# Kernel optimization log

Hardware: AMD Instinct MI355X
Metric: run time of the kernel (lower is better)

Reference implementation:

```python
import jax, jax.numpy as jnp
import numpy as np

# Sizes (match input_specs)
B = 50                 # number of CRN graphs in the batch
NS_PER, NR_PER = 2000, 4000
N_S, N_R = B * NS_PER, B * NR_PER   # 100k species, 200k reactions total
E = 1_000_000          # bipartite edges
D = 128                # d_model
L = 2                  # n_layers
N_TYPES, P_DIM = 16, 8
MAX_SPECIES_IDX = 2000


def setup_inputs() -> dict:
    key = jax.random.key(0)
    ks = jax.random.split(key, 12)
    inp = {
        "species_indices": jax.random.randint(ks[0], (N_S,), 0, MAX_SPECIES_IDX, dtype=jnp.int32),
        "is_external": jax.random.randint(ks[1], (N_S,), 0, 2, dtype=jnp.int32),
        "propensity_type_ids": jax.random.randint(ks[2], (N_R,), 0, N_TYPES, dtype=jnp.int32),
        "propensity_params": jax.random.normal(ks[3], (N_R, P_DIM), dtype=jnp.float32),
        "edge_species": jax.random.randint(ks[4], (E,), 0, N_S, dtype=jnp.int32),
        "edge_reaction": jax.random.randint(ks[5], (E,), 0, N_R, dtype=jnp.int32),
        # contiguous per-graph segment ids (graphs are equal-sized)
        "species_batch": jnp.repeat(jnp.arange(B, dtype=jnp.int32), NS_PER),
        "reaction_batch": jnp.repeat(jnp.arange(B, dtype=jnp.int32), NR_PER),
        # learned parameters
        "species_table": jax.random.normal(ks[6], (MAX_SPECIES_IDX, D), dtype=jnp.float32) * 0.02,
        "external_table": jax.random.normal(ks[7], (2, D), dtype=jnp.float32) * 0.02,
        "type_table": jax.random.normal(ks[8], (N_TYPES, D), dtype=jnp.float32) * 0.02,
        "W_param": jax.random.normal(ks[9], (P_DIM, D), dtype=jnp.float32) * 0.1,
        "b_param": jnp.zeros((D,), dtype=jnp.float32),
        # per-layer message-passing weights: concat([h, msg]) -> d
        "Wr": jax.random.normal(ks[10], (L, 2 * D, D), dtype=jnp.float32) * 0.05,
        "br": jnp.zeros((L, D), dtype=jnp.float32),
        "Ws": jax.random.normal(ks[11], (L, 2 * D, D), dtype=jnp.float32) * 0.05,
        "bs": jnp.zeros((L, D), dtype=jnp.float32),
    }
    return inp


def reference(species_indices, is_external, propensity_type_ids, propensity_params,
              edge_species, edge_reaction, species_batch, reaction_batch,
              species_table, external_table, type_table, W_param, b_param,
              Wr, br, Ws, bs):
    # Initial embeddings
    h_s = species_table[species_indices] + external_table[is_external]          # (N_S, D)
    h_r = type_table[propensity_type_ids] + propensity_params @ W_param + b_param  # (N_R, D)

    n_s, n_r = h_s.shape[0], h_r.shape[0]
    # Alternating bipartite sum message passing (SumMessagePassingLayer)
    for l in range(Wr.shape[0]):
        m_r = jax.ops.segment_sum(h_s[edge_species], edge_reaction, num_segments=n_r)
        h_r = jax.nn.relu(jnp.concatenate([h_r, m_r], axis=-1) @ Wr[l] + br[l])
        m_s = jax.ops.segment_sum(h_r[edge_reaction], edge_species, num_segments=n_s)
        h_s = jax.nn.relu(jnp.concatenate([h_s, m_s], axis=-1) @ Ws[l] + bs[l])

    # Segment-mean pooling per graph (index_add then divide by counts)
    pooled_s = jax.ops.segment_sum(h_s, species_batch, num_segments=B) / float(NS_PER)
    pooled_r = jax.ops.segment_sum(h_r, reaction_batch, num_segments=B) / float(NR_PER)
    context = jnp.concatenate([pooled_s, pooled_r], axis=-1)  # (B, 2D); dropout p=0 -> identity
    return context
```

## Files before the change

kernel.cpp:

```cpp
#include <hip/hip_runtime.h>
#include <stdint.h>

#define NS 100000
#define NR 200000
#define EE 1000000
#define DD 128
#define NB 50
#define NSP 2000
#define NRP 4000
#define BSH 10
#define NBR 196
#define NBS 98
#define CHUNK 8192

typedef short bf16x8 __attribute__((ext_vector_type(8)));
typedef float f32x4 __attribute__((ext_vector_type(4)));
typedef unsigned u32x4 __attribute__((ext_vector_type(4)));
typedef unsigned u32x2 __attribute__((ext_vector_type(2)));

__device__ __forceinline__ unsigned short f2bf(float f){
  unsigned u = __float_as_uint(f);
  u = (u + 0x7FFFu + ((u >> 16) & 1u)) >> 16;
  return (unsigned short)u;
}
__device__ __forceinline__ float bf2f(unsigned short s){
  return __uint_as_float(((unsigned)s) << 16);
}
__device__ __forceinline__ unsigned packbf(float a, float b){
  return (unsigned)f2bf(a) | ((unsigned)f2bf(b) << 16);
}
__device__ __forceinline__ float bflo(unsigned p){ return __uint_as_float(p << 16); }
__device__ __forceinline__ float bfhi(unsigned p){ return __uint_as_float(p & 0xFFFF0000u); }

__global__ void pack_w(const float* __restrict__ Wr, const float* __restrict__ Ws,
                       unsigned short* __restrict__ Wp){
  int g = blockIdx.x*256 + threadIdx.x;
  if (g >= 4*32768) return;
  int j = g & 7; int rest = g >> 3;
  int lane = rest & 63; rest >>= 6;
  int ks = rest & 7; rest >>= 3;
  int ct = rest & 7; int mat = rest >> 3;
  int k  = ks*32 + (lane >> 4)*8 + j;
  int cc = ct*16 + (lane & 15);
  const float* src = (mat < 2) ? (Wr + (size_t)mat*256*DD) : (Ws + (size_t)(mat-2)*256*DD);
  Wp[g] = f2bf(src[(size_t)k*DD + cc]);
}

__global__ __launch_bounds__(256) void init_all(const int* __restrict__ si, const int* __restrict__ ext,
        const int* __restrict__ tid, const float* __restrict__ pp,
        const float* __restrict__ st, const float* __restrict__ et, const float* __restrict__ tt,
        const float* __restrict__ Wpar, const float* __restrict__ bpar,
        unsigned short* __restrict__ hs, unsigned short* __restrict__ hr){
  int g = blockIdx.x*256 + threadIdx.x;
  int row = g >> 4, colb = (g & 15) * 8;
  if (row < NS){
    const float* a = st + (size_t)si[row]*DD + colb;
    const float* b = et + (size_t)ext[row]*DD + colb;
    float4 x0 = ((const float4*)a)[0], x1 = ((const float4*)a)[1];
    float4 y0 = ((const float4*)b)[0], y1 = ((const float4*)b)[1];
    u32x4 o;
    o.x = packbf(x0.x+y0.x, x0.y+y0.y);
    o.y = packbf(x0.z+y0.z, x0.w+y0.w);
    o.z = packbf(x1.x+y1.x, x1.y+y1.y);
    o.w = packbf(x1.z+y1.z, x1.w+y1.w);
    *(u32x4*)(hs + (size_t)row*DD + colb) = o;
  } else {
    int r = row - NS;
    const float* tb = tt + (size_t)tid[r]*DD + colb;
    float4 a0 = ((const float4*)tb)[0], a1 = ((const float4*)tb)[1];
    float4 b0 = ((const float4*)(bpar+colb))[0], b1 = ((const float4*)(bpar+colb))[1];
    a0.x += b0.x; a0.y += b0.y; a0.z += b0.z; a0.w += b0.w;
    a1.x += b1.x; a1.y += b1.y; a1.z += b1.z; a1.w += b1.w;
    const float* pr = pp + (size_t)r*8;
    float4 p0 = ((const float4*)pr)[0], p1 = ((const float4*)pr)[1];
    float w[8] = {p0.x,p0.y,p0.z,p0.w,p1.x,p1.y,p1.z,p1.w};
    #pragma unroll
    for (int p = 0; p < 8; p++){
      float4 w0 = ((const float4*)(Wpar + p*DD + colb))[0];
      float4 w1 = ((const float4*)(Wpar + p*DD + colb))[1];
      a0.x += w[p]*w0.x; a0.y += w[p]*w0.y; a0.z += w[p]*w0.z; a0.w += w[p]*w0.w;
      a1.x += w[p]*w1.x; a1.y += w[p]*w1.y; a1.z += w[p]*w1.z; a1.w += w[p]*w1.w;
    }
    u32x4 o;
    o.x = packbf(a0.x, a0.y); o.y = packbf(a0.z, a0.w);
    o.z = packbf(a1.x, a1.y); o.w = packbf(a1.z, a1.w);
    *(u32x4*)(hr + (size_t)r*DD + colb) = o;
  }
}

__global__ __launch_bounds__(256) void bucket_hist(const int* __restrict__ er, const int* __restrict__ es,
                                                   int* __restrict__ gcnt){
  __shared__ int cnt[NBR + NBS];
  int t = threadIdx.x;
  for (int j = t; j < NBR + NBS; j += 256) cnt[j] = 0;
  __syncthreads();
  long i0 = (long)blockIdx.x * 2048;
  for (int j = t; j < 2048; j += 256){
    long i = i0 + j;
    if (i < EE){
      atomicAdd(&cnt[er[i] >> BSH], 1);
      atomicAdd(&cnt[NBR + (es[i] >> BSH)], 1);
    }
  }
  __syncthreads();
  for (int j = t; j < NBR + NBS; j += 256)
    if (cnt[j]) atomicAdd(&gcnt[j], cnt[j]);
}

__global__ __launch_bounds__(256) void bucket_scan(const int* __restrict__ gcnt,
        int* __restrict__ bktOffR, int* __restrict__ bktOffS,
        int* __restrict__ gCurR, int* __restrict__ gCurS){
  __shared__ int a[256];
  int t = threadIdx.x;
  int own = (t < NBR) ? gcnt[t] : 0;
  a[t] = own; __syncthreads();
  for (int d = 1; d < 256; d <<= 1){
    int x = (t >= d) ? a[t-d] : 0;
    __syncthreads(); a[t] += x; __syncthreads();
  }
  if (t < NBR){ int v = a[t] - own; bktOffR[t] = v; gCurR[t] = v; }
  if (t == 0) bktOffR[NBR] = EE;
  __syncthreads();
  own = (t < NBS) ? gcnt[NBR + t] : 0;
  a[t] = own; __syncthreads();
  for (int d = 1; d < 256; d <<= 1){
    int x = (t >= d) ? a[t-d] : 0;
    __syncthreads(); a[t] += x; __syncthreads();
  }
  if (t < NBS){ int v = a[t] - own; bktOffS[t] = v; gCurS[t] = v; }
  if (t == 0) bktOffS[NBS] = EE;
}

__global__ __launch_bounds__(256) void bin_edges(const int* __restrict__ er, const int* __restrict__ es,
        int* __restrict__ gCurR, int* __restrict__ gCurS,
        unsigned* __restrict__ recR, unsigned* __restrict__ recS){
  __shared__ unsigned stage[CHUNK];
  __shared__ unsigned char stageb[CHUNK];
  __shared__ int cnt[256], scn[256], pref[256], gbase[256], lcur[256];
  int t = threadIdx.x;
  int side = blockIdx.y;
  const int* dest = side ? es : er;
  const int* srca = side ? er : es;
  int* gCur = side ? gCurS : gCurR;
  unsigned* rec = side ? recS : recR;
  int nbkt = side ? NBS : NBR;
  long i0 = (long)blockIdx.x * CHUNK;
  int n = (EE - i0 < CHUNK) ? (int)(EE - i0) : CHUNK;
  cnt[t] = 0;
  __syncthreads();
  for (int j = t; j < n; j += 256)
    atomicAdd(&cnt[dest[i0 + j] >> BSH], 1);
  __syncthreads();
  scn[t] = cnt[t];
  __syncthreads();
  for (int d = 1; d < 256; d <<= 1){
    int x = (t >= d) ? scn[t-d] : 0;
    __syncthreads(); scn[t] += x; __syncthreads();
  }
  pref[t] = scn[t] - cnt[t];
  lcur[t] = scn[t] - cnt[t];
  if (t < nbkt && cnt[t] > 0) gbase[t] = atomicAdd(&gCur[t], cnt[t]);
  __syncthreads();
  for (int j = t; j < n; j += 256){
    int d = dest[i0 + j];
    int s = srca[i0 + j];
    int b = d >> BSH;
    int p = atomicAdd(&lcur[b], 1);
    stage[p] = ((unsigned)(d - (b << BSH)) << 18) | (unsigned)s;
    stageb[p] = (unsigned char)b;
  }
  __syncthreads();
  for (int e = t; e < n; e += 256){
    int b = stageb[e];
    rec[gbase[b] + (e - pref[b])] = stage[e];
  }
}

__global__ __launch_bounds__(256) void build_csr(const unsigned* __restrict__ recR, const unsigned* __restrict__ recS,
        const int* __restrict__ bktOffR, const int* __restrict__ bktOffS,
        unsigned* __restrict__ csrR, unsigned* __restrict__ csrS,
        int* __restrict__ offsR, int* __restrict__ offsS){
  __shared__ int hist[1024], pref[1024], cur[1024], ws[256];
  int t = threadIdx.x;
  int bb = blockIdx.x;
  const unsigned* rec; const int* bktOff; unsigned* csr; int* offs; int N;
  if (bb < NBR){ rec = recR; bktOff = bktOffR; csr = csrR; offs = offsR; N = NR; }
  else { bb -= NBR; rec = recS; bktOff = bktOffS; csr = csrS; offs = offsS; N = NS; }
  int d0 = bb << BSH;
  int base = bktOff[bb], cnt_ = bktOff[bb+1] - base;
  #pragma unroll
  for (int j = 0; j < 4; j++) hist[t*4+j] = 0;
  __syncthreads();
  for (int e = t; e < cnt_; e += 256)
    atomicAdd(&hist[rec[base + e] >> 18], 1);
  __syncthreads();
  int s = 0, h[4];
  #pragma unroll
  for (int j = 0; j < 4; j++){ h[j] = hist[t*4+j]; s += h[j]; }
  ws[t] = s;
  __syncthreads();
  for (int d = 1; d < 256; d <<= 1){
    int x = (t >= d) ? ws[t-d] : 0;
    __syncthreads(); ws[t] += x; __syncthreads();
  }
  int run = ws[t] - s;
  #pragma unroll
  for (int j = 0; j < 4; j++){ pref[t*4+j] = run; cur[t*4+j] = base + run; run += h[j]; }
  __syncthreads();
  int DPB = N - d0; if (DPB > 1024) DPB = 1024;
  #pragma unroll
  for (int j = 0; j < 4; j++){
    int i = t*4 + j;
    if (i < DPB) offs[d0 + i] = base + pref[i];
  }
  if (t == 0 && d0 + DPB == N) offs[N] = EE;
  __syncthreads();
  for (int e = t; e < cnt_; e += 256){
    unsigned r = rec[base + e];
    int pos = atomicAdd(&cur[r >> 18], 1);
    csr[pos] = (((r >> 18) & 31u) << 26) | ((r & 0x3FFFFu) << 8);
  }
}

__global__ __launch_bounds__(256) void fused_layer(
        const unsigned short* __restrict__ gsrc,
        const unsigned short* __restrict__ hself,
        const int* __restrict__ offs, const unsigned* __restrict__ csr,
        const unsigned short* __restrict__ Wp, const float* __restrict__ bias,
        unsigned short* __restrict__ hout)
{
  __shared__ unsigned short msgT[32*DD];
  int t = threadIdx.x;
  int lane = t & 63;
  int w = t >> 6;
  int quad = lane >> 4, rlo = lane & 15;
  int row0 = blockIdx.x * 32;

  for (int i = t; i < 2048; i += 256) ((unsigned*)msgT)[i] = 0u;
  __syncthreads();

  {
    int rbeg = row0 + w*8;
    int k  = __builtin_amdgcn_readfirstlane(offs[rbeg]);
    int ke = __builtin_amdgcn_readfirstlane(offs[rbeg + 8]);
    int c16 = lane >> 2, sub4 = lane & 3;
    const char* gbase = (const char*)gsrc;
    float a0 = 0.f, a1 = 0.f;
    int cur = -1;
    unsigned rc[8]; unsigned pv[8];
    if (k < ke){
      #pragma unroll
      for (int i = 0; i < 8; i++){
        int kk = (k + i < ke) ? (k + i) : (ke - 1);
        rc[i] = (unsigned)__builtin_amdgcn_readfirstlane(csr[kk]);
      }
      #pragma unroll
      for (int i = 0; i < 8; i++)
        pv[i] = *(const unsigned*)(gbase + (rc[i] & 0x03FFFF00u) + lane*4);
      while (k < ke){
        unsigned rc2[8], pv2[8];
        int kn = k + 8;
        #pragma unroll
        for (int i = 0; i < 8; i++){
          int kk = (kn + i < ke) ? (kn + i) : (ke - 1);
          rc2[i] = (unsigned)__builtin_amdgcn_readfirstlane(csr[kk]);
        }
        #pragma unroll
        for (int i = 0; i < 8; i++)
          pv2[i] = *(const unsigned*)(gbase + (rc2[i] & 0x03FFFF00u) + lane*4);
        #pragma unroll
        for (int i = 0; i < 8; i++){
          if (k + i < ke){
            int dl = (int)(rc[i] >> 26);
            if (dl != cur){
              if (cur >= 0)
                *(unsigned*)(msgT + cur*DD + ((c16 ^ (cur & 7)) << 3) + (sub4 << 1)) = packbf(a0, a1);
              a0 = 0.f; a1 = 0.f;
              cur = dl;
            }
            a0 += bflo(pv[i]); a1 += bfhi(pv[i]);
          }
        }
        #pragma unroll
        for (int i = 0; i < 8; i++){ rc[i] = rc2[i]; pv[i] = pv2[i]; }
        k = kn;
      }
      if (cur >= 0)
        *(unsigned*)(msgT + cur*DD + ((c16 ^ (cur & 7)) << 3) + (sub4 << 1)) = packbf(a0, a1);
    }
  }
  __syncthreads();

  int ct0 = w * 2;
  bf16x8 wf[16];
  #pragma unroll
  for (int ks = 0; ks < 8; ks++){
    wf[ks*2+0] = *(const bf16x8*)(Wp + (size_t)(((ct0+0)*8 + ks)*64 + lane) * 8);
    wf[ks*2+1] = *(const bf16x8*)(Wp + (size_t)(((ct0+1)*8 + ks)*64 + lane) * 8);
  }
  bf16x8 Hb0[4], Hb1[4];
  #pragma unroll
  for (int ks = 0; ks < 4; ks++){
    int kloc = ks*32 + quad*8;
    Hb0[ks] = *(const bf16x8*)(hself + (size_t)(row0 + rlo) * DD + kloc);
    Hb1[ks] = *(const bf16x8*)(hself + (size_t)(row0 + 16 + rlo) * DD + kloc);
  }
  bf16x8 Mb0[4], Mb1[4];
  #pragma unroll
  for (int ks2 = 0; ks2 < 4; ks2++){
    int c8 = ks2*4 + quad;
    int lr0 = rlo, lr1 = 16 + rlo;
    Mb0[ks2] = *(const bf16x8*)(msgT + lr0*DD + ((c8 ^ (lr0 & 7)) * 8));
    Mb1[ks2] = *(const bf16x8*)(msgT + lr1*DD + ((c8 ^ (lr1 & 7)) * 8));
  }

  f32x4 acc[2][2];
  #pragma unroll
  for (int i = 0; i < 2; i++)
    #pragma unroll
    for (int j = 0; j < 2; j++){ f32x4 z = {0.f,0.f,0.f,0.f}; acc[i][j] = z; }

  #pragma unroll
  for (int ks = 0; ks < 4; ks++){
    acc[0][0] = __builtin_amdgcn_mfma_f32_16x16x32_bf16(wf[ks*2+0], Hb0[ks], acc[0][0], 0, 0, 0);
    acc[0][1] = __builtin_amdgcn_mfma_f32_16x16x32_bf16(wf[ks*2+1], Hb0[ks], acc[0][1], 0, 0, 0);
    acc[1][0] = __builtin_amdgcn_mfma_f32_16x16x32_bf16(wf[ks*2+0], Hb1[ks], acc[1][0], 0, 0, 0);
    acc[1][1] = __builtin_amdgcn_mfma_f32_16x16x32_bf16(wf[ks*2+1], Hb1[ks], acc[1][1], 0, 0, 0);
  }
  #pragma unroll
  for (int ks2 = 0; ks2 < 4; ks2++){
    int ks = 4 + ks2;
    acc[0][0] = __builtin_amdgcn_mfma_f32_16x16x32_bf16(wf[ks*2+0], Mb0[ks2], acc[0][0], 0, 0, 0);
    acc[0][1] = __builtin_amdgcn_mfma_f32_16x16x32_bf16(wf[ks*2+1], Mb0[ks2], acc[0][1], 0, 0, 0);
    acc[1][0] = __builtin_amdgcn_mfma_f32_16x16x32_bf16(wf[ks*2+0], Mb1[ks2], acc[1][0], 0, 0, 0);
    acc[1][1] = __builtin_amdgcn_mfma_f32_16x16x32_bf16(wf[ks*2+1], Mb1[ks2], acc[1][1], 0, 0, 0);
  }

  #pragma unroll
  for (int c = 0; c < 2; c++){
    float4 bv = *(const float4*)(bias + (ct0+c)*16 + quad*4);
    #pragma unroll
    for (int rb = 0; rb < 2; rb++){
      int row = row0 + rb*16 + rlo;
      float v0 = acc[rb][c][0] + bv.x;
      float v1 = acc[rb][c][1] + bv.y;
      float v2 = acc[rb][c][2] + bv.z;
      float v3 = acc[rb][c][3] + bv.w;
      v0 = v0 > 0.f ? v0 : 0.f;
      v1 = v1 > 0.f ? v1 : 0.f;
      v2 = v2 > 0.f ? v2 : 0.f;
      v3 = v3 > 0.f ? v3 : 0.f;
      u32x2 o; o.x = packbf(v0, v1); o.y = packbf(v2, v3);
      *(u32x2*)(hout + (size_t)row*DD + (ct0+c)*16 + quad*4) = o;
    }
  }
}

__global__ __launch_bounds__(256) void pool(const unsigned short* __restrict__ hs,
        const unsigned short* __restrict__ hr, float* __restrict__ out){
  __shared__ float red[16][128];
  int b = blockIdx.x, part = blockIdx.y;
  int t = threadIdx.x;
  int rg = t >> 4, sub = t & 15;
  const unsigned short* src; int row0, outoff; float scale;
  if (part < 4){ src = hs; row0 = b*NSP + part*500; outoff = b*256; scale = 1.f/NSP; }
  else { src = hr; row0 = b*NRP + (part-4)*500; outoff = b*256 + 128; scale = 1.f/NRP; }
  float a0=0,a1=0,a2=0,a3=0,a4=0,a5=0,a6=0,a7=0;
  for (int r = rg; r < 500; r += 16){
    u32x4 p = *(const u32x4*)(src + (size_t)(row0+r)*DD + sub*8);
    a0 += bflo(p.x); a1 += bfhi(p.x);
    a2 += bflo(p.y); a3 += bfhi(p.y);
    a4 += bflo(p.z); a5 += bfhi(p.z);
    a6 += bflo(p.w); a7 += bfhi(p.w);
  }
  float* rr = &red[rg][sub*8];
  rr[0]=a0; rr[1]=a1; rr[2]=a2; rr[3]=a3; rr[4]=a4; rr[5]=a5; rr[6]=a6; rr[7]=a7;
  __syncthreads();
  if (t < 128){
    float s = 0.f;
    #pragma unroll
    for (int g = 0; g < 16; g++) s += red[g][t];
    atomicAdd(&out[outoff + t], s * scale);
  }
}

extern "C" void kernel_launch(void* const* d_in, const int* in_sizes, int n_in,
                              void* d_out, int out_size, void* d_ws, size_t ws_size,
                              hipStream_t stream)
{
  const int*   si   = (const int*)d_in[0];
  const int*   ext  = (const int*)d_in[1];
  const int*   tid  = (const int*)d_in[2];
  const float* pp   = (const float*)d_in[3];
  const int*   es   = (const int*)d_in[4];
  const int*   er   = (const int*)d_in[5];
  const float* st   = (const float*)d_in[8];
  const float* et   = (const float*)d_in[9];
  const float* tt   = (const float*)d_in[10];
  const float* Wpar = (const float*)d_in[11];
  const float* bpar = (const float*)d_in[12];
  const float* Wr   = (const float*)d_in[13];
  const float* br   = (const float*)d_in[14];
  const float* Ws   = (const float*)d_in[15];
  const float* bs   = (const float*)d_in[16];
  float* out = (float*)d_out;

  char* basep = (char*)d_ws; size_t off = 0;
  auto alloc = [&](size_t bytes)->char*{
    char* r = basep + off; off = (off + bytes + 255) & ~(size_t)255; return r;
  };
  unsigned short* hs0 = (unsigned short*)alloc((size_t)NS*DD*2);
  unsigned short* hs1 = (unsigned short*)alloc((size_t)NS*DD*2);
  unsigned short* hr0 = (unsigned short*)alloc((size_t)NR*DD*2);
  unsigned short* hr1 = (unsigned short*)alloc((size_t)NR*DD*2);
  unsigned short* Wp  = (unsigned short*)alloc((size_t)4*32768*2);
  int* offsR = (int*)alloc((size_t)(NR+1)*4);
  int* offsS = (int*)alloc((size_t)(NS+1)*4);
  unsigned* csrR = (unsigned*)alloc((size_t)EE*4);
  unsigned* csrS = (unsigned*)alloc((size_t)EE*4);
  int* gcnt   = (int*)alloc(2048);
  int* bktOffR= (int*)alloc(2048);
  int* bktOffS= (int*)alloc(2048);
  int* gCurR  = (int*)alloc(2048);
  int* gCurS  = (int*)alloc(2048);
  unsigned* recR = (unsigned*)hs1;
  unsigned* recS = (unsigned*)hr1;

  hipMemsetAsync(gcnt, 0, 2048, stream);
  hipMemsetAsync(d_out, 0, (size_t)out_size*4, stream);

  pack_w<<<512, 256, 0, stream>>>(Wr, Ws, Wp);
  init_all<<<(NS+NR)*16/256, 256, 0, stream>>>(si, ext, tid, pp, st, et, tt, Wpar, bpar, hs0, hr0);

  bucket_hist<<<(EE + 2047)/2048, 256, 0, stream>>>(er, es, gcnt);
  bucket_scan<<<1, 256, 0, stream>>>(gcnt, bktOffR, bktOffS, gCurR, gCurS);
  bin_edges<<<dim3((EE + CHUNK - 1)/CHUNK, 2), 256, 0, stream>>>(er, es, gCurR, gCurS, recR, recS);
  build_csr<<<NBR + NBS, 256, 0, stream>>>(recR, recS, bktOffR, bktOffS, csrR, csrS, offsR, offsS);

  fused_layer<<<NR/32, 256, 0, stream>>>(hs0, hr0, offsR, csrR, Wp + (size_t)0*32768, br + (size_t)0*DD, hr1);
  fused_layer<<<NS/32, 256, 0, stream>>>(hr1, hs0, offsS, csrS, Wp + (size_t)2*32768, bs + (size_t)0*DD, hs1);
  fused_layer<<<NR/32, 256, 0, stream>>>(hs1, hr1, offsR, csrR, Wp + (size_t)1*32768, br + (size_t)1*DD, hr0);
  fused_layer<<<NS/32, 256, 0, stream>>>(hr0, hs1, offsS, csrS, Wp + (size_t)3*32768, bs + (size_t)1*DD, hs0);

  pool<<<dim3(NB, 12), 256, 0, stream>>>(hs0, hr0, out);
}
```

Before: 463.2 us.

## Pad CSR rows to even length and gather two edges per wave

CSR construction is split into a histogram kernel, a serial pad-scan kernel and a scatter kernel. Each destination's edge list is padded to an even length with a dummy edge that points at an extra zeroed row appended to each feature buffer. In the fused layer, the two half-waves then load 8-byte slices from two different source rows at once and combine partial sums with a cross-half shuffle before writing to LDS. The goal is fewer loop iterations and wider gather loads. The cost is three extra launches, four small memsets, a single-threaded scan, and extra padded edges to gather.

```diff
diff --git a/kernel.cpp b/kernel.cpp
--- a/kernel.cpp
+++ b/kernel.cpp
@@ -22,9 +22,6 @@
   unsigned u = __float_as_uint(f);
   u = (u + 0x7FFFu + ((u >> 16) & 1u)) >> 16;
   return (unsigned short)u;
-}
-__device__ __forceinline__ float bf2f(unsigned short s){
-  return __uint_as_float(((unsigned)s) << 16);
 }
 __device__ __forceinline__ unsigned packbf(float a, float b){
   return (unsigned)f2bf(a) | ((unsigned)f2bf(b) << 16);
@@ -176,49 +173,89 @@
   }
 }
 
-__global__ __launch_bounds__(256) void build_csr(const unsigned* __restrict__ recR, const unsigned* __restrict__ recS,
+__global__ __launch_bounds__(256) void csr_hist(const unsigned* __restrict__ recR, const unsigned* __restrict__ recS,
         const int* __restrict__ bktOffR, const int* __restrict__ bktOffS,
-        unsigned* __restrict__ csrR, unsigned* __restrict__ csrS,
-        int* __restrict__ offsR, int* __restrict__ offsS){
-  __shared__ int hist[1024], pref[1024], cur[1024], ws[256];
-  int t = threadIdx.x;
-  int bb = blockIdx.x;
-  const unsigned* rec; const int* bktOff; unsigned* csr; int* offs; int N;
-  if (bb < NBR){ rec = recR; bktOff = bktOffR; csr = csrR; offs = offsR; N = NR; }
-  else { bb -= NBR; rec = recS; bktOff = bktOffS; csr = csrS; offs = offsS; N = NS; }
-  int d0 = bb << BSH;
-  int base = bktOff[bb], cnt_ = bktOff[bb+1] - base;
+        int* __restrict__ histBuf, int* __restrict__ gPad){
+  __shared__ int hist[1024]; __shared__ int ws[256];
+  int t = threadIdx.x; int bb = blockIdx.x;
+  const unsigned* rec; const int* bktOff; int lb;
+  if (bb < NBR){ rec = recR; bktOff = bktOffR; lb = bb; }
+  else { rec = recS; bktOff = bktOffS; lb = bb - NBR; }
+  int base = bktOff[lb], cnt_ = bktOff[lb+1] - base;
   #pragma unroll
   for (int j = 0; j < 4; j++) hist[t*4+j] = 0;
   __syncthreads();
   for (int e = t; e < cnt_; e += 256)
     atomicAdd(&hist[rec[base + e] >> 18], 1);
   __syncthreads();
-  int s = 0, h[4];
-  #pragma unroll
-  for (int j = 0; j < 4; j++){ h[j] = hist[t*4+j]; s += h[j]; }
-  ws[t] = s;
-  __syncthreads();
+  int s = 0;
+  #pragma unroll
+  for (int j = 0; j < 4; j++){
+    int h = hist[t*4+j];
+    histBuf[bb*1024 + t*4 + j] = h;
+    s += h + (h & 1);
+  }
+  ws[t] = s; __syncthreads();
   for (int d = 1; d < 256; d <<= 1){
     int x = (t >= d) ? ws[t-d] : 0;
     __syncthreads(); ws[t] += x; __syncthreads();
   }
-  int run = ws[t] - s;
-  #pragma unroll
-  for (int j = 0; j < 4; j++){ pref[t*4+j] = run; cur[t*4+j] = base + run; run += h[j]; }
-  __syncthreads();
+  if (t == 255) gPad[bb] = ws[255];
+}
+
+__global__ void padscan(const int* __restrict__ gPad, int* __restrict__ padBase){
+  if (threadIdx.x == 0 && blockIdx.x == 0){
+    int b = 0;
+    for (int i = 0; i < NBR; i++){ padBase[i] = b; b += gPad[i]; }
+    padBase[NBR] = b;
+    b = 0;
+    for (int i = 0; i < NBS; i++){ padBase[256 + i] = b; b += gPad[NBR + i]; }
+    padBase[256 + NBS] = b;
+  }
+}
+
+__global__ __launch_bounds__(256) void csr_scatter(const unsigned* __restrict__ recR, const unsigned* __restrict__ recS,
+        const int* __restrict__ bktOffR, const int* __restrict__ bktOffS,
+        const int* __restrict__ histBuf, const int* __restrict__ padBase,
+        unsigned* __restrict__ csrR, unsigned* __restrict__ csrS,
+        int* __restrict__ offsR, int* __restrict__ offsS){
+  __shared__ int cur[1024], ws[256];
+  int t = threadIdx.x; int bb = blockIdx.x;
+  const unsigned* rec; const int* bktOff; unsigned* csr; int* offs; int N, lb, pbase; unsigned zrow;
+  if (bb < NBR){ rec = recR; bktOff = bktOffR; csr = csrR; offs = offsR; N = NR; lb = bb;
+                 pbase = padBase[bb]; zrow = NS; }
+  else { lb = bb - NBR; rec = recS; bktOff = bktOffS; csr = csrS; offs = offsS; N = NS;
+         pbase = padBase[256 + lb]; zrow = NR; }
+  int d0 = lb << BSH;
+  int base = bktOff[lb], cnt_ = bktOff[lb+1] - base;
+  int h[4], s = 0;
+  #pragma unroll
+  for (int j = 0; j < 4; j++){ h[j] = histBuf[bb*1024 + t*4 + j]; s += h[j] + (h[j] & 1); }
+  ws[t] = s; __syncthreads();
+  for (int d = 1; d < 256; d <<= 1){
+    int x = (t >= d) ? ws[t-d] : 0;
+    __syncthreads(); ws[t] += x; __syncthreads();
+  }
+  int run = pbase + ws[t] - s;
   int DPB = N - d0; if (DPB > 1024) DPB = 1024;
   #pragma unroll
   for (int j = 0; j < 4; j++){
     int i = t*4 + j;
-    if (i < DPB) offs[d0 + i] = base + pref[i];
-  }
-  if (t == 0 && d0 + DPB == N) offs[N] = EE;
+    cur[i] = run;
+    if (i < DPB){
+      offs[d0 + i] = run;
+      if (h[j] & 1) csr[run + h[j]] = ((unsigned)(i & 31) << 26) | (zrow << 8);
+    }
+    run += h[j] + (h[j] & 1);
+  }
+  if (t == 0 && d0 + DPB == N)
+    offs[N] = (N == NR) ? padBase[NBR] : padBase[256 + NBS];
   __syncthreads();
   for (int e = t; e < cnt_; e += 256){
     unsigned r = rec[base + e];
-    int pos = atomicAdd(&cur[r >> 18], 1);
-    csr[pos] = (((r >> 18) & 31u) << 26) | ((r & 0x3FFFFu) << 8);
+    int dloc10 = r >> 18;
+    int pos = atomicAdd(&cur[dloc10], 1);
+    csr[pos] = ((unsigned)(dloc10 & 31) << 26) | ((r & 0x3FFFFu) << 8);
   }
 }
 
@@ -243,22 +280,37 @@
     int rbeg = row0 + w*8;
     int k  = __builtin_amdgcn_readfirstlane(offs[rbeg]);
     int ke = __builtin_amdgcn_readfirstlane(offs[rbeg + 8]);
-    int c16 = lane >> 2, sub4 = lane & 3;
+    int half = lane >> 5, col4 = lane & 31;
     const char* gbase = (const char*)gsrc;
-    float a0 = 0.f, a1 = 0.f;
+    float a0 = 0.f, a1 = 0.f, a2 = 0.f, a3 = 0.f;
     int cur = -1;
-    unsigned rc[8]; unsigned pv[8];
+
+    auto flushrow = [&](){
+      float s0 = a0 + __shfl_xor(a0, 32, 64);
+      float s1 = a1 + __shfl_xor(a1, 32, 64);
+      float s2 = a2 + __shfl_xor(a2, 32, 64);
+      float s3 = a3 + __shfl_xor(a3, 32, 64);
+      if (lane < 32){
+        u32x2 o; o.x = packbf(s0, s1); o.y = packbf(s2, s3);
+        *(u32x2*)(msgT + cur*DD + (((col4 >> 1) ^ (cur & 7)) * 8) + ((col4 & 1) * 4)) = o;
+      }
+      a0 = 0.f; a1 = 0.f; a2 = 0.f; a3 = 0.f;
+    };
+
     if (k < ke){
+      unsigned rc[8]; u32x2 pv[4];
       #pragma unroll
       for (int i = 0; i < 8; i++){
         int kk = (k + i < ke) ? (k + i) : (ke - 1);
         rc[i] = (unsigned)__builtin_amdgcn_readfirstlane(csr[kk]);
       }
       #pragma unroll
-      for (int i = 0; i < 8; i++)
-        pv[i] = *(const unsigned*)(gbase + (rc[i] & 0x03FFFF00u) + lane*4);
+      for (int j = 0; j < 4; j++){
+        unsigned rsel = half ? rc[2*j+1] : rc[2*j];
+        pv[j] = *(const u32x2*)(gbase + (rsel & 0x03FFFF00u) + col4*8);
+      }
       while (k < ke){
-        unsigned rc2[8], pv2[8];
+        unsigned rc2[8]; u32x2 pv2[4];
         int kn = k + 8;
         #pragma unroll
         for (int i = 0; i < 8; i++){
@@ -266,27 +318,29 @@
           rc2[i] = (unsigned)__builtin_amdgcn_readfirstlane(csr[kk]);
         }
         #pragma unroll
-        for (int i = 0; i < 8; i++)
-          pv2[i] = *(const unsigned*)(gbase + (rc2[i] & 0x03FFFF00u) + lane*4);
+        for (int j = 0; j < 4; j++){
+          unsigned rsel = half ? rc2[2*j+1] : rc2[2*j];
+          pv2[j] = *(const u32x2*)(gbase + (rsel & 0x03FFFF00u) + col4*8);
+        }
         #pragma unroll
-        for (int i = 0; i < 8; i++){
-          if (k + i < ke){
-            int dl = (int)(rc[i] >> 26);
+        for (int j = 0; j < 4; j++){
+          if (k + 2*j < ke){
+            int dl = (int)(rc[2*j] >> 26);
             if (dl != cur){
-              if (cur >= 0)
-                *(unsigned*)(msgT + cur*DD + ((c16 ^ (cur & 7)) << 3) + (sub4 << 1)) = packbf(a0, a1);
-              a0 = 0.f; a1 = 0.f;
+              if (cur >= 0) flushrow();
               cur = dl;
             }
-            a0 += bflo(pv[i]); a1 += bfhi(pv[i]);
+            a0 += bflo(pv[j].x); a1 += bfhi(pv[j].x);
+            a2 += bflo(pv[j].y); a3 += bfhi(pv[j].y);
           }
         }
         #pragma unroll
-        for (int i = 0; i < 8; i++){ rc[i] = rc2[i]; pv[i] = pv2[i]; }
+        for (int i = 0; i < 8; i++) rc[i] = rc2[i];
+        #pragma unroll
+        for (int j = 0; j < 4; j++) pv[j] = pv2[j];
         k = kn;
       }
-      if (cur >= 0)
-        *(unsigned*)(msgT + cur*DD + ((c16 ^ (cur & 7)) << 3) + (sub4 << 1)) = packbf(a0, a1);
+      if (cur >= 0) flushrow();
     }
   }
   __syncthreads();
@@ -409,25 +463,32 @@
   auto alloc = [&](size_t bytes)->char*{
     char* r = basep + off; off = (off + bytes + 255) & ~(size_t)255; return r;
   };
-  unsigned short* hs0 = (unsigned short*)alloc((size_t)NS*DD*2);
-  unsigned short* hs1 = (unsigned short*)alloc((size_t)NS*DD*2);
-  unsigned short* hr0 = (unsigned short*)alloc((size_t)NR*DD*2);
-  unsigned short* hr1 = (unsigned short*)alloc((size_t)NR*DD*2);
+  unsigned short* hs0 = (unsigned short*)alloc((size_t)(NS+1)*DD*2);
+  unsigned short* hs1 = (unsigned short*)alloc((size_t)(NS+1)*DD*2);
+  unsigned short* hr0 = (unsigned short*)alloc((size_t)(NR+1)*DD*2);
+  unsigned short* hr1 = (unsigned short*)alloc((size_t)(NR+1)*DD*2);
   unsigned short* Wp  = (unsigned short*)alloc((size_t)4*32768*2);
   int* offsR = (int*)alloc((size_t)(NR+1)*4);
   int* offsS = (int*)alloc((size_t)(NS+1)*4);
-  unsigned* csrR = (unsigned*)alloc((size_t)EE*4);
-  unsigned* csrS = (unsigned*)alloc((size_t)EE*4);
+  unsigned* csrR = (unsigned*)alloc((size_t)(EE+NR+64)*4);
+  unsigned* csrS = (unsigned*)alloc((size_t)(EE+NS+64)*4);
+  int* histBuf = (int*)alloc((size_t)(NBR+NBS)*1024*4);
   int* gcnt   = (int*)alloc(2048);
   int* bktOffR= (int*)alloc(2048);
   int* bktOffS= (int*)alloc(2048);
   int* gCurR  = (int*)alloc(2048);
   int* gCurS  = (int*)alloc(2048);
+  int* gPad   = (int*)alloc(2048);
+  int* padBase= (int*)alloc(2048);
   unsigned* recR = (unsigned*)hs1;
   unsigned* recS = (unsigned*)hr1;
 
   hipMemsetAsync(gcnt, 0, 2048, stream);
   hipMemsetAsync(d_out, 0, (size_t)out_size*4, stream);
+  hipMemsetAsync(hs0 + (size_t)NS*DD, 0, DD*2, stream);
+  hipMemsetAsync(hs1 + (size_t)NS*DD, 0, DD*2, stream);
+  hipMemsetAsync(hr0 + (size_t)NR*DD, 0, DD*2, stream);
+  hipMemsetAsync(hr1 + (size_t)NR*DD, 0, DD*2, stream);
 
   pack_w<<<512, 256, 0, stream>>>(Wr, Ws, Wp);
   init_all<<<(NS+NR)*16/256, 256, 0, stream>>>(si, ext, tid, pp, st, et, tt, Wpar, bpar, hs0, hr0);
@@ -435,7 +496,10 @@
   bucket_hist<<<(EE + 2047)/2048, 256, 0, stream>>>(er, es, gcnt);
   bucket_scan<<<1, 256, 0, stream>>>(gcnt, bktOffR, bktOffS, gCurR, gCurS);
   bin_edges<<<dim3((EE + CHUNK - 1)/CHUNK, 2), 256, 0, stream>>>(er, es, gCurR, gCurS, recR, recS);
-  build_csr<<<NBR + NBS, 256, 0, stream>>>(recR, recS, bktOffR, bktOffS, csrR, csrS, offsR, offsS);
+  csr_hist<<<NBR + NBS, 256, 0, stream>>>(recR, recS, bktOffR, bktOffS, histBuf, gPad);
+  padscan<<<1, 64, 0, stream>>>(gPad, padBase);
+  csr_scatter<<<NBR + NBS, 256, 0, stream>>>(recR, recS, bktOffR, bktOffS, histBuf, padBase,
+                                             csrR, csrS, offsR, offsS);
 
   fused_layer<<<NR/32, 256, 0, stream>>>(hs0, hr0, offsR, csrR, Wp + (size_t)0*32768, br + (size_t)0*DD, hr1);
   fused_layer<<<NS/32, 256, 0, stream>>>(hr1, hs0, offsS, csrS, Wp + (size_t)2*32768, bs + (size_t)0*DD, hs1);
```

New measurement: 560.0 us. 1.21x slower.
